# Optimization experiments

Hardware: AMD Instinct MI355X
Metric: run time of the kernel (lower is better)

The kernel has to match this reference:

```python
import jax, jax.numpy as jnp
import numpy as np

N_SRC = 50000   # source nodes in the block
N_DST = 50000   # destination nodes
E = 800000      # edges (avg in-degree 16, every dst has >=1 edge)
D = 256         # hidden_dim
V = 50000       # vocab_size
C = 104         # n_classes (POJ-104)


def setup_inputs() -> dict:
    key = jax.random.key(0)
    k1, k2, k3, k4, k5, k6 = jax.random.split(key, 6)
    token_id = jax.random.randint(k1, (N_SRC,), 0, V, dtype=jnp.int32)
    src_idx = jax.random.randint(k2, (E,), 0, N_SRC, dtype=jnp.int32)
    # every dst node gets at least one in-edge (DGL raises on 0-in-degree),
    # remaining edges land on random dst nodes; sorted so edges are grouped by dst
    extra = jax.random.randint(k3, (E - N_DST,), 0, N_DST, dtype=jnp.int32)
    dst_idx = jnp.sort(jnp.concatenate([jnp.arange(N_DST, dtype=jnp.int32), extra]))
    emb = jax.random.normal(k4, (V, D), dtype=jnp.float32)  # nn.Embedding default N(0,1)
    W = jax.random.normal(k5, (D, D), dtype=jnp.float32) / jnp.sqrt(D)
    b = jnp.zeros((D,), dtype=jnp.float32)
    Wc = jax.random.normal(k6, (C, D), dtype=jnp.float32) / jnp.sqrt(D)
    bc = jnp.zeros((C,), dtype=jnp.float32)
    return {"emb": emb, "W": W, "b": b, "Wc": Wc, "bc": bc,
            "token_id": token_id, "src_idx": src_idx, "dst_idx": dst_idx}


def reference(emb, W, b, Wc, bc, token_id, src_idx, dst_idx):
    # embedding gather for source nodes (first_layer branch)
    feat_src = emb[token_id]                  # [N_SRC, D]
    # message: copy_u -> mailbox messages per edge
    msgs = feat_src[src_idx]                  # [E, D]
    # per-dst segment stats (dst_idx is sorted / grouped by dst)
    deg = jax.ops.segment_sum(jnp.ones((E,), dtype=jnp.int32), dst_idx,
                              num_segments=N_DST)            # [N_DST]
    sum_all = jax.ops.segment_sum(msgs, dst_idx, num_segments=N_DST)  # [N_DST, D]
    # DGL mailbox reducer: last message in the segment is the 'current input',
    # the rest are children summed through CodeRNNCell: x = cur + relu(W @ sum_children + b)
    last_idx = jnp.cumsum(deg) - 1            # index of last edge per dst segment
    last_msg = msgs[last_idx]                 # [N_DST, D]
    child_sum = sum_all - last_msg            # sum of msgs excluding the last one
    rnn_out = last_msg + jax.nn.relu(child_sum @ W.T + b)
    # length == 1 segments bypass the RNN cell entirely: ft = the single message
    ft = jnp.where((deg == 1)[:, None], last_msg, rnn_out)   # [N_DST, D]
    # final classifier
    return ft @ Wc.T + bc                     # [N_DST, C]
```

## Files before the change

kernel.cpp:

```cpp
#include <hip/hip_runtime.h>
#include <hip/hip_bf16.h>

#define DD 256
#define CC 104
#define NSL 8

typedef __bf16 bf16x8 __attribute__((ext_vector_type(8)));
typedef float  f32x4  __attribute__((ext_vector_type(4)));

__device__ inline float bu2f(unsigned short u) {
    return __uint_as_float(((unsigned)u) << 16);
}
__device__ inline unsigned short f2bu(float f) {
    __hip_bfloat16 h = __float2bfloat16(f);
    return *reinterpret_cast<unsigned short*>(&h);
}

__global__ void prep_all(
    const int* __restrict__ token_id,
    const int* __restrict__ src_idx,
    const int* __restrict__ dst_idx,
    int* __restrict__ seg_start,
    int* __restrict__ seg_end,
    int* __restrict__ edge_tok,
    int* __restrict__ last_tok,
    int E, int PB,
    const float* __restrict__ W,
    const float* __restrict__ Wc,
    __hip_bfloat16* __restrict__ Wfrag,
    __hip_bfloat16* __restrict__ Wcfrag)
{
    const int b = blockIdx.x;
    const int t = threadIdx.x;
    if (b < PB) {
        int e = b * 256 + t;
        if (e >= E) return;
        int d = dst_idx[e];
        int tok = token_id[src_idx[e]];
        edge_tok[e] = tok;
        if (e == 0 || dst_idx[e - 1] != d) seg_start[d] = e;
        if (e == E - 1 || dst_idx[e + 1] != d) { seg_end[d] = e + 1; last_tok[d] = tok; }
        return;
    }
    if (b < PB + 32) {
        int idx  = (b - PB) * 256 + t;
        int lane = idx & 63, g = idx >> 6;
        int nt = g & 15, k0 = g >> 4;
        int r = nt * 16 + (lane & 15);
        int c = k0 * 32 + (lane >> 4) * 8;
        const float* src = W + (size_t)r * DD + c;
        float4 v0 = *(const float4*)(src);
        float4 v1 = *(const float4*)(src + 4);
        uint4 pk;
        pk.x = (unsigned)f2bu(v0.x) | ((unsigned)f2bu(v0.y) << 16);
        pk.y = (unsigned)f2bu(v0.z) | ((unsigned)f2bu(v0.w) << 16);
        pk.z = (unsigned)f2bu(v1.x) | ((unsigned)f2bu(v1.y) << 16);
        pk.w = (unsigned)f2bu(v1.z) | ((unsigned)f2bu(v1.w) << 16);
        *(uint4*)(Wfrag + (size_t)idx * 8) = pk;
        return;
    }
    {
        int idx  = (b - PB - 32) * 256 + t;
        int lane = idx & 63, g = idx >> 6;
        int nt = g & 7, k0 = g >> 3;
        int r = nt * 16 + (lane & 15);
        int c = k0 * 32 + (lane >> 4) * 8;
        float4 v0 = make_float4(0.f,0.f,0.f,0.f);
        float4 v1 = make_float4(0.f,0.f,0.f,0.f);
        if (r < CC) {
            const float* src = Wc + (size_t)r * DD + c;
            v0 = *(const float4*)(src);
            v1 = *(const float4*)(src + 4);
        }
        uint4 pk;
        pk.x = (unsigned)f2bu(v0.x) | ((unsigned)f2bu(v0.y) << 16);
        pk.y = (unsigned)f2bu(v0.z) | ((unsigned)f2bu(v0.w) << 16);
        pk.z = (unsigned)f2bu(v1.x) | ((unsigned)f2bu(v1.y) << 16);
        pk.w = (unsigned)f2bu(v1.z) | ((unsigned)f2bu(v1.w) << 16);
        *(uint4*)(Wcfrag + (size_t)idx * 8) = pk;
    }
}

__global__ __launch_bounds__(256, 3) void we_gemm(
    const float* __restrict__ emb,
    const __hip_bfloat16* __restrict__ Wfrag,
    __hip_bfloat16* __restrict__ Webuf,
    __hip_bfloat16* __restrict__ embb,
    int V)
{
    __shared__ __hip_bfloat16 lds[32 * 512];
    const int t    = threadIdx.x;
    const int lane = t & 63;
    const int w    = t >> 6;
    const int quad = lane >> 4;
    const int l16  = lane & 15;
    const int mrow = blockIdx.x * 64 + w * 16 + l16;
    const int row  = min(mrow, V - 1);

    bf16x8 bfrag[8];
#pragma unroll
    for (int k0 = 0; k0 < 8; ++k0) {
        const float* src = emb + (size_t)row * DD + k0 * 32 + quad * 8;
        float4 v0 = *(const float4*)(src);
        float4 v1 = *(const float4*)(src + 4);
        uint4 pk;
        pk.x = (unsigned)f2bu(v0.x) | ((unsigned)f2bu(v0.y) << 16);
        pk.y = (unsigned)f2bu(v0.z) | ((unsigned)f2bu(v0.w) << 16);
        pk.z = (unsigned)f2bu(v1.x) | ((unsigned)f2bu(v1.y) << 16);
        pk.w = (unsigned)f2bu(v1.z) | ((unsigned)f2bu(v1.w) << 16);
        bfrag[k0] = *(bf16x8*)&pk;
        if (mrow < V)
            *(uint4*)(embb + (size_t)k0 * V * 32 + (size_t)row * 32 + quad * 8) = pk;
    }

    f32x4 acc[16];
#pragma unroll
    for (int nt = 0; nt < 16; ++nt) acc[nt] = (f32x4){0.f,0.f,0.f,0.f};

    for (int p = 0; p < 4; ++p) {
        if (p) __syncthreads();
#pragma unroll
        for (int it = 0; it < 8; ++it) {
            int idx = it * 256 + t;
            *(uint4*)(lds + (size_t)idx * 8) =
                *(const uint4*)(Wfrag + (size_t)p * 16384 + (size_t)idx * 8);
        }
        __syncthreads();
#pragma unroll
        for (int kl = 0; kl < 2; ++kl) {
            int k0 = p * 2 + kl;
#pragma unroll
            for (int nt = 0; nt < 16; ++nt) {
                bf16x8 wf = *(const bf16x8*)(lds + (kl * 16 + nt) * 512 + lane * 8);
                acc[nt] = __builtin_amdgcn_mfma_f32_16x16x32_bf16(wf, bfrag[k0], acc[nt], 0, 0, 0);
            }
        }
    }

    if (mrow < V) {
#pragma unroll
        for (int nt = 0; nt < 16; ++nt) {
            int c0 = nt * 16 + quad * 4;
            ushort4 o;
            o.x = f2bu(acc[nt][0]);
            o.y = f2bu(acc[nt][1]);
            o.z = f2bu(acc[nt][2]);
            o.w = f2bu(acc[nt][3]);
            *(ushort4*)(Webuf + (size_t)(c0 >> 5) * V * 32 +
                        (size_t)mrow * 32 + (c0 & 31)) = o;
        }
    }
}

__global__ __launch_bounds__(256, 8) void seg_rnn_kernel(
    const __hip_bfloat16* __restrict__ Webuf,
    const __hip_bfloat16* __restrict__ embb,
    const int* __restrict__ edge_tok,
    const int* __restrict__ seg_start,
    const int* __restrict__ seg_end,
    const int* __restrict__ last_tok,
    const float* __restrict__ bvec,
    __hip_bfloat16* __restrict__ ftb,
    int n_dst, int V)
{
    const int bid  = blockIdx.x;
    const int sl   = bid & 7;
    const int g    = bid >> 3;
    const int t    = threadIdx.x;
    const int wv   = t >> 6;
    const int lane = t & 63;
    const int grp  = lane >> 2;
    const int c    = lane & 3;

    int d = g * 64 + wv * 16 + grp;
    bool dok = d < n_dst;
    int dc = dok ? d : n_dst - 1;
    int s  = seg_start[dc];
    int e  = seg_end[dc];
    int lt = last_tok[dc];
    int n  = dok ? (e - 1 - s) : 0;

    const __hip_bfloat16* wsl = Webuf + (size_t)sl * V * 32;
    const __hip_bfloat16* esl = embb  + (size_t)sl * V * 32;
    uint4 lm = *(const uint4*)(esl + (size_t)lt * 32 + c * 8);

    float acc[8] = {0.f,0.f,0.f,0.f,0.f,0.f,0.f,0.f};

    for (int j = 0; ; j += 2) {
        bool a0 = j < n, a1 = j + 1 < n;
        if (!__any(a0)) break;
        uint4 u0 = make_uint4(0u,0u,0u,0u);
        uint4 u1 = make_uint4(0u,0u,0u,0u);
        if (a0) {
            int t0 = edge_tok[s + j];
            u0 = *(const uint4*)(wsl + (size_t)t0 * 32 + c * 8);
        }
        if (a1) {
            int t1 = edge_tok[s + j + 1];
            u1 = *(const uint4*)(wsl + (size_t)t1 * 32 + c * 8);
        }
        const unsigned* p0 = (const unsigned*)&u0;
        const unsigned* p1 = (const unsigned*)&u1;
#pragma unroll
        for (int k = 0; k < 4; ++k) {
            acc[2*k]   += __uint_as_float(p0[k] << 16)
                        + __uint_as_float(p1[k] << 16);
            acc[2*k+1] += __uint_as_float(p0[k] & 0xffff0000u)
                        + __uint_as_float(p1[k] & 0xffff0000u);
        }
    }

    bool gate = n > 0;
    float4 b0 = *(const float4*)(bvec + sl * 32 + c * 8);
    float4 b1 = *(const float4*)(bvec + sl * 32 + c * 8 + 4);
    float bl[8] = {b0.x, b0.y, b0.z, b0.w, b1.x, b1.y, b1.z, b1.w};
    const unsigned* lmd = (const unsigned*)&lm;
    uint4 o;
    unsigned* od = (unsigned*)&o;
#pragma unroll
    for (int k = 0; k < 4; ++k) {
        float lo = __uint_as_float(lmd[k] << 16);
        float hi = __uint_as_float(lmd[k] & 0xffff0000u);
        float v0 = lo + (gate ? fmaxf(acc[2*k]   + bl[2*k],   0.f) : 0.f);
        float v1 = hi + (gate ? fmaxf(acc[2*k+1] + bl[2*k+1], 0.f) : 0.f);
        od[k] = (unsigned)f2bu(v0) | ((unsigned)f2bu(v1) << 16);
    }
    if (dok)
        *(uint4*)(ftb + (size_t)sl * n_dst * 32 + (size_t)d * 32 + c * 8) = o;
}

__global__ __launch_bounds__(256, 4) void cls_mfma(
    const __hip_bfloat16* __restrict__ ftb,
    const __hip_bfloat16* __restrict__ Wcfrag,
    const float* __restrict__ bc,
    float* __restrict__ out,
    int M)
{
    __shared__ __hip_bfloat16 lds[32 * 512];
    const int t    = threadIdx.x;
    const int lane = t & 63;
    const int w    = t >> 6;
    const int quad = lane >> 4;
    const int l16  = lane & 15;
    const int mw   = blockIdx.x * 64 + w * 16;

    int mrow = min(mw + l16, M - 1);
    bf16x8 ffrag[8];
#pragma unroll
    for (int k0 = 0; k0 < 8; ++k0)
        ffrag[k0] = *(const bf16x8*)(ftb + (size_t)k0 * M * 32 +
                                     (size_t)mrow * 32 + quad * 8);

    f32x4 acc[8];
#pragma unroll
    for (int nt = 0; nt < 8; ++nt) acc[nt] = (f32x4){0.f,0.f,0.f,0.f};

    for (int p = 0; p < 2; ++p) {
        if (p) __syncthreads();
#pragma unroll
        for (int it = 0; it < 8; ++it) {
            int idx = it * 256 + t;
            *(uint4*)(lds + (size_t)idx * 8) =
                *(const uint4*)(Wcfrag + (size_t)p * 16384 + (size_t)idx * 8);
        }
        __syncthreads();
#pragma unroll
        for (int kl = 0; kl < 4; ++kl) {
            int k0 = p * 4 + kl;
#pragma unroll
            for (int nt = 0; nt < 8; ++nt) {
                bf16x8 wf = *(const bf16x8*)(lds + (kl * 8 + nt) * 512 + lane * 8);
                acc[nt] = __builtin_amdgcn_mfma_f32_16x16x32_bf16(wf, ffrag[k0], acc[nt], 0, 0, 0);
            }
        }
    }

    int m = mw + l16;
    if (m < M) {
#pragma unroll
        for (int nt = 0; nt < 8; ++nt) {
            int c0 = nt * 16 + quad * 4;
            if (c0 <= 100) {
                float4 bia = *(const float4*)(bc + c0);
                float4 o;
                o.x = acc[nt][0] + bia.x;
                o.y = acc[nt][1] + bia.y;
                o.z = acc[nt][2] + bia.z;
                o.w = acc[nt][3] + bia.w;
                *(float4*)(out + (size_t)m * CC + c0) = o;
            }
        }
    }
}

extern "C" void kernel_launch(void* const* d_in, const int* in_sizes, int n_in,
                              void* d_out, int out_size, void* d_ws, size_t ws_size,
                              hipStream_t stream)
{
    const float* emb      = (const float*)d_in[0];
    const float* W        = (const float*)d_in[1];
    const float* bvec     = (const float*)d_in[2];
    const float* Wc       = (const float*)d_in[3];
    const float* bc       = (const float*)d_in[4];
    const int*   token_id = (const int*)d_in[5];
    const int*   src_idx  = (const int*)d_in[6];
    const int*   dst_idx  = (const int*)d_in[7];
    float*       out      = (float*)d_out;

    const int E     = in_sizes[6];
    const int Vemb  = in_sizes[0] / DD;
    const int n_dst = out_size / CC;
    (void)n_in; (void)ws_size;

    char* ws = (char*)d_ws;
    size_t off = 0;
    auto alloc = [&](size_t bytes) {
        void* p = ws + off;
        off = (off + bytes + 255) & ~(size_t)255;
        return p;
    };
    int* seg_start = (int*)alloc((size_t)n_dst * sizeof(int));
    int* seg_end   = (int*)alloc((size_t)n_dst * sizeof(int));
    int* last_tok  = (int*)alloc((size_t)n_dst * sizeof(int));
    int* edge_tok  = (int*)alloc((size_t)E * sizeof(int));
    __hip_bfloat16* embb   = (__hip_bfloat16*)alloc((size_t)Vemb * DD * 2);
    __hip_bfloat16* Webuf  = (__hip_bfloat16*)alloc((size_t)Vemb * DD * 2);
    __hip_bfloat16* ftb    = (__hip_bfloat16*)alloc((size_t)n_dst * DD * 2);
    __hip_bfloat16* Wfrag  = (__hip_bfloat16*)alloc((size_t)128 * 512 * 2);
    __hip_bfloat16* Wcfrag = (__hip_bfloat16*)alloc((size_t)64 * 512 * 2);

    const int PB = (E + 255) / 256;
    const int we_blocks  = (Vemb + 63) / 64;
    const int seg_blocks = NSL * ((n_dst + 63) / 64);
    const int cls_blocks = (n_dst + 63) / 64;

    prep_all<<<PB + 48, 256, 0, stream>>>(
        token_id, src_idx, dst_idx, seg_start, seg_end, edge_tok, last_tok, E, PB,
        W, Wc, Wfrag, Wcfrag);
    we_gemm<<<we_blocks, 256, 0, stream>>>(
        emb, Wfrag, Webuf, embb, Vemb);
    seg_rnn_kernel<<<seg_blocks, 256, 0, stream>>>(
        Webuf, embb, edge_tok, seg_start, seg_end, last_tok, bvec, ftb,
        n_dst, Vemb);
    cls_mfma<<<cls_blocks, 256, 0, stream>>>(
        ftb, Wcfrag, bc, out, n_dst);
}
```

Measured before the change: 199.9 us.

## Replace per-destination gather-sum with MFMA one-hot segment reduction

The segment-sum kernel is rewritten. Each wave handles 16 consecutive destinations, streams their contiguous edge range 32 edges at a time into LDS, and reduces them with bf16 MFMA against a one-hot selection matrix built from a per-edge packed code (token, low dst bits, last-edge flag). This replaces a per-lane serial loop with divergent segment lengths, aiming for coalesced contiguous edge loads and balanced work. In exchange it adds LDS traffic, assumes token ids fit in 16 bits, and the LDS write/read sequence within a wave has no explicit barrier. It also runs with lower occupancy (launch bounds drop from 8 to 4).

```diff
diff --git a/kernel.cpp b/kernel.cpp
--- a/kernel.cpp
+++ b/kernel.cpp
@@ -22,7 +22,7 @@
     const int* __restrict__ dst_idx,
     int* __restrict__ seg_start,
     int* __restrict__ seg_end,
-    int* __restrict__ edge_tok,
+    int* __restrict__ etp,
     int* __restrict__ last_tok,
     int E, int PB,
     const float* __restrict__ W,
@@ -37,9 +37,10 @@
         if (e >= E) return;
         int d = dst_idx[e];
         int tok = token_id[src_idx[e]];
-        edge_tok[e] = tok;
+        int lastf = (e == E - 1 || dst_idx[e + 1] != d) ? 1 : 0;
+        etp[e] = tok | ((d & 15) << 16) | (lastf << 20);
         if (e == 0 || dst_idx[e - 1] != d) seg_start[d] = e;
-        if (e == E - 1 || dst_idx[e + 1] != d) { seg_end[d] = e + 1; last_tok[d] = tok; }
+        if (lastf) { seg_end[d] = e + 1; last_tok[d] = tok; }
         return;
     }
     if (b < PB + 32) {
@@ -152,81 +153,116 @@
     }
 }
 
-__global__ __launch_bounds__(256, 8) void seg_rnn_kernel(
+__global__ __launch_bounds__(256, 4) void seg_mfma(
     const __hip_bfloat16* __restrict__ Webuf,
     const __hip_bfloat16* __restrict__ embb,
-    const int* __restrict__ edge_tok,
+    const int* __restrict__ etp,
     const int* __restrict__ seg_start,
     const int* __restrict__ seg_end,
     const int* __restrict__ last_tok,
     const float* __restrict__ bvec,
     __hip_bfloat16* __restrict__ ftb,
-    int n_dst, int V)
-{
-    const int bid  = blockIdx.x;
-    const int sl   = bid & 7;
-    const int g    = bid >> 3;
-    const int t    = threadIdx.x;
-    const int wv   = t >> 6;
-    const int lane = t & 63;
-    const int grp  = lane >> 2;
-    const int c    = lane & 3;
-
-    int d = g * 64 + wv * 16 + grp;
-    bool dok = d < n_dst;
-    int dc = dok ? d : n_dst - 1;
-    int s  = seg_start[dc];
-    int e  = seg_end[dc];
-    int lt = last_tok[dc];
-    int n  = dok ? (e - 1 - s) : 0;
-
+    int n_dst, int V, int E)
+{
+    __shared__ unsigned char      ldsB[4][2304];
+    __shared__ unsigned long long ldsC[4][4];
+    const int t   = threadIdx.x;
+    const int wv  = t >> 6;
+    const int l   = t & 63;
+    const int sl  = blockIdx.x & 7;
+    const int g   = (blockIdx.x >> 3) * 4 + wv;
+    const int d0  = g * 16;
+    if (d0 >= n_dst) return;
+    const int d1  = min(d0 + 16, n_dst);
+    const int S   = seg_start[d0];
+    const int End = seg_end[d1 - 1];
+    const int l15 = l & 15;
+    const int kb  = (l >> 4) * 8;
+    const int k   = l >> 1;
+    const int half= l & 1;
     const __hip_bfloat16* wsl = Webuf + (size_t)sl * V * 32;
     const __hip_bfloat16* esl = embb  + (size_t)sl * V * 32;
-    uint4 lm = *(const uint4*)(esl + (size_t)lt * 32 + c * 8);
-
-    float acc[8] = {0.f,0.f,0.f,0.f,0.f,0.f,0.f,0.f};
-
-    for (int j = 0; ; j += 2) {
-        bool a0 = j < n, a1 = j + 1 < n;
-        if (!__any(a0)) break;
-        uint4 u0 = make_uint4(0u,0u,0u,0u);
-        uint4 u1 = make_uint4(0u,0u,0u,0u);
-        if (a0) {
-            int t0 = edge_tok[s + j];
-            u0 = *(const uint4*)(wsl + (size_t)t0 * 32 + c * 8);
-        }
-        if (a1) {
-            int t1 = edge_tok[s + j + 1];
-            u1 = *(const uint4*)(wsl + (size_t)t1 * 32 + c * 8);
-        }
-        const unsigned* p0 = (const unsigned*)&u0;
-        const unsigned* p1 = (const unsigned*)&u1;
-#pragma unroll
-        for (int k = 0; k < 4; ++k) {
-            acc[2*k]   += __uint_as_float(p0[k] << 16)
-                        + __uint_as_float(p1[k] << 16);
-            acc[2*k+1] += __uint_as_float(p0[k] & 0xffff0000u)
-                        + __uint_as_float(p1[k] & 0xffff0000u);
-        }
-    }
-
-    bool gate = n > 0;
-    float4 b0 = *(const float4*)(bvec + sl * 32 + c * 8);
-    float4 b1 = *(const float4*)(bvec + sl * 32 + c * 8 + 4);
-    float bl[8] = {b0.x, b0.y, b0.z, b0.w, b1.x, b1.y, b1.z, b1.w};
-    const unsigned* lmd = (const unsigned*)&lm;
-    uint4 o;
-    unsigned* od = (unsigned*)&o;
-#pragma unroll
-    for (int k = 0; k < 4; ++k) {
-        float lo = __uint_as_float(lmd[k] << 16);
-        float hi = __uint_as_float(lmd[k] & 0xffff0000u);
-        float v0 = lo + (gate ? fmaxf(acc[2*k]   + bl[2*k],   0.f) : 0.f);
-        float v1 = hi + (gate ? fmaxf(acc[2*k+1] + bl[2*k+1], 0.f) : 0.f);
-        od[k] = (unsigned)f2bu(v0) | ((unsigned)f2bu(v1) << 16);
-    }
-    if (dok)
-        *(uint4*)(ftb + (size_t)sl * n_dst * 32 + (size_t)d * 32 + c * 8) = o;
+    unsigned char*      myB = ldsB[wv];
+    unsigned long long* myC = ldsC[wv];
+
+    f32x4 acc0 = {0.f,0.f,0.f,0.f};
+    f32x4 acc1 = {0.f,0.f,0.f,0.f};
+    const int R = (End - S + 31) >> 5;
+
+    for (int r = 0; r < R; ++r) {
+        int e  = S + 32 * r + k;
+        int ec = min(e, End - 1);
+        int m  = etp[ec];
+        int tok = m & 0xFFFF;
+        const __hip_bfloat16* src = wsl + (size_t)tok * 32 + half * 16;
+        uint4 Q0 = *(const uint4*)(src);
+        uint4 Q1 = *(const uint4*)(src + 8);
+        unsigned char* dstB = myB + k * 72 + half * 32;
+        *(uint2*)(dstB)      = make_uint2(Q0.x, Q0.y);
+        *(uint2*)(dstB + 8)  = make_uint2(Q0.z, Q0.w);
+        *(uint2*)(dstB + 16) = make_uint2(Q1.x, Q1.y);
+        *(uint2*)(dstB + 24) = make_uint2(Q1.z, Q1.w);
+        int code = (e < End && !((m >> 20) & 1)) ? ((m >> 16) & 15) : 255;
+        if (half == 0) ((unsigned char*)myC)[k] = (unsigned char)code;
+        unsigned long long c8 = myC[l >> 4];
+        unsigned mw0, mw1, mw2, mw3;
+        {
+            unsigned ul15 = (unsigned)l15;
+            mw0 = (((unsigned)(c8 >>  0) & 0xFFu) == ul15 ? 0x3F80u : 0u)
+                | (((unsigned)(c8 >>  8) & 0xFFu) == ul15 ? 0x3F800000u : 0u);
+            mw1 = (((unsigned)(c8 >> 16) & 0xFFu) == ul15 ? 0x3F80u : 0u)
+                | (((unsigned)(c8 >> 24) & 0xFFu) == ul15 ? 0x3F800000u : 0u);
+            mw2 = (((unsigned)(c8 >> 32) & 0xFFu) == ul15 ? 0x3F80u : 0u)
+                | (((unsigned)(c8 >> 40) & 0xFFu) == ul15 ? 0x3F800000u : 0u);
+            mw3 = (((unsigned)(c8 >> 48) & 0xFFu) == ul15 ? 0x3F80u : 0u)
+                | (((unsigned)(c8 >> 56) & 0xFFu) == ul15 ? 0x3F800000u : 0u);
+        }
+        uint4 mq = make_uint4(mw0, mw1, mw2, mw3);
+        bf16x8 bm = *(bf16x8*)&mq;
+#pragma unroll
+        for (int h = 0; h < 2; ++h) {
+            const unsigned char* ab = myB + h * 32 + l15 * 2;
+            unsigned aw0, aw1, aw2, aw3;
+            aw0 = (unsigned)*(const unsigned short*)(ab + (kb + 0) * 72)
+                | ((unsigned)*(const unsigned short*)(ab + (kb + 1) * 72) << 16);
+            aw1 = (unsigned)*(const unsigned short*)(ab + (kb + 2) * 72)
+                | ((unsigned)*(const unsigned short*)(ab + (kb + 3) * 72) << 16);
+            aw2 = (unsigned)*(const unsigned short*)(ab + (kb + 4) * 72)
+                | ((unsigned)*(const unsigned short*)(ab + (kb + 5) * 72) << 16);
+            aw3 = (unsigned)*(const unsigned short*)(ab + (kb + 6) * 72)
+                | ((unsigned)*(const unsigned short*)(ab + (kb + 7) * 72) << 16);
+            uint4 aq = make_uint4(aw0, aw1, aw2, aw3);
+            bf16x8 am = *(bf16x8*)&aq;
+            if (h == 0) acc0 = __builtin_amdgcn_mfma_f32_16x16x32_bf16(am, bm, acc0, 0, 0, 0);
+            else        acc1 = __builtin_amdgcn_mfma_f32_16x16x32_bf16(am, bm, acc1, 0, 0, 0);
+        }
+    }
+
+    int dst = d0 + l15;
+    bool dok = dst < n_dst;
+    int dc = min(dst, n_dst - 1);
+    int lt  = last_tok[dc];
+    int nch = seg_end[dc] - seg_start[dc] - 1;
+    bool gate = nch > 0;
+    int q = (l >> 4) * 4;
+    ushort4 lm0 = *(const ushort4*)(esl + (size_t)lt * 32 + q);
+    ushort4 lm1 = *(const ushort4*)(esl + (size_t)lt * 32 + 16 + q);
+    float4 b0 = *(const float4*)(bvec + sl * 32 + q);
+    float4 b1 = *(const float4*)(bvec + sl * 32 + 16 + q);
+    ushort4 o0, o1;
+    o0.x = f2bu(bu2f(lm0.x) + (gate ? fmaxf(acc0[0] + b0.x, 0.f) : 0.f));
+    o0.y = f2bu(bu2f(lm0.y) + (gate ? fmaxf(acc0[1] + b0.y, 0.f) : 0.f));
+    o0.z = f2bu(bu2f(lm0.z) + (gate ? fmaxf(acc0[2] + b0.z, 0.f) : 0.f));
+    o0.w = f2bu(bu2f(lm0.w) + (gate ? fmaxf(acc0[3] + b0.w, 0.f) : 0.f));
+    o1.x = f2bu(bu2f(lm1.x) + (gate ? fmaxf(acc1[0] + b1.x, 0.f) : 0.f));
+    o1.y = f2bu(bu2f(lm1.y) + (gate ? fmaxf(acc1[1] + b1.y, 0.f) : 0.f));
+    o1.z = f2bu(bu2f(lm1.z) + (gate ? fmaxf(acc1[2] + b1.z, 0.f) : 0.f));
+    o1.w = f2bu(bu2f(lm1.w) + (gate ? fmaxf(acc1[3] + b1.w, 0.f) : 0.f));
+    if (dok) {
+        __hip_bfloat16* fb = ftb + (size_t)sl * n_dst * 32 + (size_t)dst * 32;
+        *(ushort4*)(fb + q)      = o0;
+        *(ushort4*)(fb + 16 + q) = o1;
+    }
 }
 
 __global__ __launch_bounds__(256, 4) void cls_mfma(
@@ -322,7 +358,7 @@
     int* seg_start = (int*)alloc((size_t)n_dst * sizeof(int));
     int* seg_end   = (int*)alloc((size_t)n_dst * sizeof(int));
     int* last_tok  = (int*)alloc((size_t)n_dst * sizeof(int));
-    int* edge_tok  = (int*)alloc((size_t)E * sizeof(int));
+    int* etp       = (int*)alloc((size_t)E * sizeof(int));
     __hip_bfloat16* embb   = (__hip_bfloat16*)alloc((size_t)Vemb * DD * 2);
     __hip_bfloat16* Webuf  = (__hip_bfloat16*)alloc((size_t)Vemb * DD * 2);
     __hip_bfloat16* ftb    = (__hip_bfloat16*)alloc((size_t)n_dst * DD * 2);
@@ -331,17 +367,18 @@
 
     const int PB = (E + 255) / 256;
     const int we_blocks  = (Vemb + 63) / 64;
-    const int seg_blocks = NSL * ((n_dst + 63) / 64);
+    const int ngroups    = (n_dst + 15) / 16;
+    const int seg_blocks = NSL * ((ngroups + 3) / 4);
     const int cls_blocks = (n_dst + 63) / 64;
 
     prep_all<<<PB + 48, 256, 0, stream>>>(
-        token_id, src_idx, dst_idx, seg_start, seg_end, edge_tok, last_tok, E, PB,
+        token_id, src_idx, dst_idx, seg_start, seg_end, etp, last_tok, E, PB,
         W, Wc, Wfrag, Wcfrag);
     we_gemm<<<we_blocks, 256, 0, stream>>>(
         emb, Wfrag, Webuf, embb, Vemb);
-    seg_rnn_kernel<<<seg_blocks, 256, 0, stream>>>(
-        Webuf, embb, edge_tok, seg_start, seg_end, last_tok, bvec, ftb,
-        n_dst, Vemb);
+    seg_mfma<<<seg_blocks, 256, 0, stream>>>(
+        Webuf, embb, etp, seg_start, seg_end, last_tok, bvec, ftb,
+        n_dst, Vemb, E);
     cls_mfma<<<cls_blocks, 256, 0, stream>>>(
         ftb, Wcfrag, bc, out, n_dst);
 }
```

New measurement: 188.0 us. 1.06x faster.
